# Optimization experiments

Measured on AMD Instinct MI355X. Metric: run time of the kernel, lower is better.

Reference implementation:

```python
import jax, jax.numpy as jnp
import numpy as np

B = 1048576
NUM_USERS = 200000
NUM_ITEMS = 100000
NUM_GROUPS = 50000
D = 32  # embedding_dim; grp_forward hardcodes 4*32 reshape -> 3 members per group


def setup_inputs() -> dict:
    key = jax.random.key(0)
    ks = jax.random.split(key, 12)
    return {
        "group_inputs": jax.random.randint(ks[0], (B,), 0, NUM_GROUPS, dtype=jnp.int32),
        "item_inputs": jax.random.randint(ks[1], (B,), 0, NUM_ITEMS, dtype=jnp.int32),
        "group_members": jax.random.randint(ks[2], (NUM_GROUPS, 3), 0, NUM_USERS, dtype=jnp.int32),
        "user_emb": jax.random.normal(ks[3], (NUM_USERS, D), dtype=jnp.float32) * 0.1,
        "item_emb": jax.random.normal(ks[4], (NUM_ITEMS, D), dtype=jnp.float32) * 0.1,
        "att_w1": jax.random.normal(ks[5], (4 * D, 16), dtype=jnp.float32) * 0.1,
        "att_b1": jnp.zeros((16,), dtype=jnp.float32),
        "att_w2": jax.random.normal(ks[6], (16, 3), dtype=jnp.float32) * 0.1,
        "att_b2": jnp.zeros((3,), dtype=jnp.float32),
        "pred_w1": jax.random.normal(ks[7], (3 * D, 8), dtype=jnp.float32) * 0.1,
        "pred_b1": jnp.zeros((8,), dtype=jnp.float32),
        "pred_w2": jax.random.normal(ks[8], (8, 1), dtype=jnp.float32) * 0.1,
        "pred_b2": jnp.zeros((1,), dtype=jnp.float32),
    }


def reference(group_inputs, item_inputs, group_members,
              user_emb, item_emb,
              att_w1, att_b1, att_w2, att_b2,
              pred_w1, pred_b1, pred_w2, pred_b2):
    # Vectorized form of AGREE.grp_forward (3 members per group, dropout=0 eval)
    members = group_members[group_inputs]            # [B, 3]
    me = user_emb[members]                            # [B, 3, D] member embeds
    ie = item_emb[item_inputs]                        # [B, D]
    # concat(members, item) along member dim, flatten to [B, 4D]
    x = jnp.concatenate([me.reshape(-1, 3 * D), ie], axis=1)  # [B, 4D]
    h = jax.nn.relu(x @ att_w1 + att_b1)              # [B, 16]
    wt = jax.nn.softmax(h @ att_w2 + att_b2, axis=1)  # [B, 3] attention weights
    g = jnp.einsum('bm,bmd->bd', wt, me)              # [B, D] attended group embed
    new = jnp.concatenate([g * ie, g, ie], axis=1)    # [B, 3D]
    h2 = jax.nn.relu(new @ pred_w1 + pred_b1)         # [B, 8]
    y = jax.nn.sigmoid(h2 @ pred_w2 + pred_b2)        # [B, 1]
    return y
```

## Files before the change

kernel.cpp:

```cpp
#include <hip/hip_runtime.h>
#include <math.h>
#include <stdint.h>

#define DD 32
#define GRECW 56
#define IRECW 24

__device__ __forceinline__ uint32_t bf16rne(float f) {
    uint32_t u = __float_as_uint(f);
    return (u + 0x7fffu + ((u >> 16) & 1u)) >> 16;
}
__device__ __forceinline__ uint32_t pack2(float a, float b) {
    return bf16rne(a) | (bf16rne(b) << 16);
}
#define BLO(u) __uint_as_float((u) << 16)
#define BHI(u) __uint_as_float((u) & 0xffff0000u)

__global__ __launch_bounds__(256) void grp_pre(
    const int* __restrict__ gm, const float* __restrict__ ue,
    const float* __restrict__ w1, const float* __restrict__ b1,
    uint32_t* __restrict__ grec, int NG)
{
    int tid = blockIdx.x * 256 + threadIdx.x;
    int g = tid >> 2, q = tid & 3;
    if (g >= NG) return;
    uint32_t* rec = grec + (size_t)g * GRECW;

    int u0 = gm[3 * g + 0], u1 = gm[3 * g + 1], u2 = gm[3 * g + 2];
    float me[96];
    {
        const float4* p0 = reinterpret_cast<const float4*>(ue + (size_t)u0 * DD);
        const float4* p1 = reinterpret_cast<const float4*>(ue + (size_t)u1 * DD);
        const float4* p2 = reinterpret_cast<const float4*>(ue + (size_t)u2 * DD);
        #pragma unroll
        for (int c = 0; c < 8; ++c) {
            float4 v0 = p0[c], v1 = p1[c], v2 = p2[c];
            me[4*c+0]    = v0.x; me[4*c+1]    = v0.y; me[4*c+2]    = v0.z; me[4*c+3]    = v0.w;
            me[32+4*c+0] = v1.x; me[32+4*c+1] = v1.y; me[32+4*c+2] = v1.z; me[32+4*c+3] = v1.w;
            me[64+4*c+0] = v2.x; me[64+4*c+1] = v2.y; me[64+4*c+2] = v2.z; me[64+4*c+3] = v2.w;
        }
    }
    float s0 = b1[4*q+0], s1 = b1[4*q+1], s2 = b1[4*q+2], s3 = b1[4*q+3];
    #pragma unroll
    for (int d = 0; d < 96; ++d) {
        float x = me[d];
        const float4 wv = *reinterpret_cast<const float4*>(w1 + d * 16 + 4 * q);
        s0 = fmaf(x, wv.x, s0);
        s1 = fmaf(x, wv.y, s1);
        s2 = fmaf(x, wv.z, s2);
        s3 = fmaf(x, wv.w, s3);
    }
    uint2 sw;
    sw.x = pack2(s0, s1);
    sw.y = pack2(s2, s3);
    *reinterpret_cast<uint2*>(rec + 2 * q) = sw;

    if (q >= 1) {
        int m = q - 1;
        const float* src = me + 32 * m;
        uint32_t* dst = rec + 8 + 16 * m;
        #pragma unroll
        for (int c = 0; c < 4; ++c) {
            uint4 o;
            o.x = pack2(src[8*c+0], src[8*c+1]);
            o.y = pack2(src[8*c+2], src[8*c+3]);
            o.z = pack2(src[8*c+4], src[8*c+5]);
            o.w = pack2(src[8*c+6], src[8*c+7]);
            *reinterpret_cast<uint4*>(dst + 4 * c) = o;
        }
    }
}

__global__ __launch_bounds__(256) void item_pre(
    const float* __restrict__ itemb, const float* __restrict__ w1,
    uint32_t* __restrict__ irec, int NI)
{
    int tid = blockIdx.x * 256 + threadIdx.x;
    int i = tid >> 1, q = tid & 1;
    if (i >= NI) return;
    uint32_t* rec = irec + (size_t)i * IRECW;

    float ev[32];
    {
        const float4* p = reinterpret_cast<const float4*>(itemb + (size_t)i * DD);
        #pragma unroll
        for (int c = 0; c < 8; ++c) {
            float4 v = p[c];
            ev[4*c+0] = v.x; ev[4*c+1] = v.y; ev[4*c+2] = v.z; ev[4*c+3] = v.w;
        }
    }
    float tt[8];
    #pragma unroll
    for (int j = 0; j < 8; ++j) tt[j] = 0.0f;
    #pragma unroll
    for (int d = 0; d < 32; ++d) {
        float x = ev[d];
        const float4 wa = *reinterpret_cast<const float4*>(w1 + (96 + d) * 16 + 8 * q);
        const float4 wb = *reinterpret_cast<const float4*>(w1 + (96 + d) * 16 + 8 * q + 4);
        tt[0] = fmaf(x, wa.x, tt[0]); tt[1] = fmaf(x, wa.y, tt[1]);
        tt[2] = fmaf(x, wa.z, tt[2]); tt[3] = fmaf(x, wa.w, tt[3]);
        tt[4] = fmaf(x, wb.x, tt[4]); tt[5] = fmaf(x, wb.y, tt[5]);
        tt[6] = fmaf(x, wb.z, tt[6]); tt[7] = fmaf(x, wb.w, tt[7]);
    }
    uint4 tw;
    tw.x = pack2(tt[0], tt[1]); tw.y = pack2(tt[2], tt[3]);
    tw.z = pack2(tt[4], tt[5]); tw.w = pack2(tt[6], tt[7]);
    *reinterpret_cast<uint4*>(rec + 4 * q) = tw;

    {
        const float* src = ev + 16 * q;
        uint32_t* dst = rec + 8 + 8 * q;
        #pragma unroll
        for (int c = 0; c < 2; ++c) {
            uint4 o;
            o.x = pack2(src[8*c+0], src[8*c+1]);
            o.y = pack2(src[8*c+2], src[8*c+3]);
            o.z = pack2(src[8*c+4], src[8*c+5]);
            o.w = pack2(src[8*c+6], src[8*c+7]);
            *reinterpret_cast<uint4*>(dst + 4 * c) = o;
        }
    }
}

__global__ __launch_bounds__(256) void agree_main(
    const int* __restrict__ gi, const int* __restrict__ ii,
    const uint32_t* __restrict__ grec, const uint32_t* __restrict__ irec,
    const float* __restrict__ w2, const float* __restrict__ b2,
    const float* __restrict__ pw1, const float* __restrict__ pb1,
    const float* __restrict__ pw2, const float* __restrict__ pb2,
    float* __restrict__ out, int B)
{
    int b = blockIdx.x * 256 + threadIdx.x;
    if (b >= B) return;

    const uint4* gr4 = reinterpret_cast<const uint4*>(grec + (size_t)gi[b] * GRECW);
    const uint4* ir4 = reinterpret_cast<const uint4*>(irec + (size_t)ii[b] * IRECW);

    uint4 G[14];
    #pragma unroll
    for (int c = 0; c < 14; ++c) G[c] = gr4[c];
    uint4 I[6];
    #pragma unroll
    for (int c = 0; c < 6; ++c) I[c] = ir4[c];

    float h[16];
    #pragma unroll
    for (int c = 0; c < 2; ++c) {
        uint4 sa = G[c];
        uint4 ta = I[c];
        h[8*c+0] = fmaxf(BLO(sa.x) + BLO(ta.x), 0.0f);
        h[8*c+1] = fmaxf(BHI(sa.x) + BHI(ta.x), 0.0f);
        h[8*c+2] = fmaxf(BLO(sa.y) + BLO(ta.y), 0.0f);
        h[8*c+3] = fmaxf(BHI(sa.y) + BHI(ta.y), 0.0f);
        h[8*c+4] = fmaxf(BLO(sa.z) + BLO(ta.z), 0.0f);
        h[8*c+5] = fmaxf(BHI(sa.z) + BHI(ta.z), 0.0f);
        h[8*c+6] = fmaxf(BLO(sa.w) + BLO(ta.w), 0.0f);
        h[8*c+7] = fmaxf(BHI(sa.w) + BHI(ta.w), 0.0f);
    }

    float l0 = b2[0], l1 = b2[1], l2 = b2[2];
    #pragma unroll
    for (int j = 0; j < 16; ++j) {
        l0 = fmaf(h[j], w2[j * 3 + 0], l0);
        l1 = fmaf(h[j], w2[j * 3 + 1], l1);
        l2 = fmaf(h[j], w2[j * 3 + 2], l2);
    }
    float mx = fmaxf(l0, fmaxf(l1, l2));
    float e0 = __expf(l0 - mx);
    float e1 = __expf(l1 - mx);
    float e2 = __expf(l2 - mx);
    float inv = 1.0f / (e0 + e1 + e2);
    float wt0 = e0 * inv, wt1 = e1 * inv, wt2 = e2 * inv;

    float g[32];
    #pragma unroll
    for (int c = 0; c < 4; ++c) {
        uint4 a  = G[2 + c];
        uint4 bq = G[6 + c];
        uint4 cq = G[10 + c];
        g[8*c+0] = fmaf(wt0, BLO(a.x), fmaf(wt1, BLO(bq.x), wt2 * BLO(cq.x)));
        g[8*c+1] = fmaf(wt0, BHI(a.x), fmaf(wt1, BHI(bq.x), wt2 * BHI(cq.x)));
        g[8*c+2] = fmaf(wt0, BLO(a.y), fmaf(wt1, BLO(bq.y), wt2 * BLO(cq.y)));
        g[8*c+3] = fmaf(wt0, BHI(a.y), fmaf(wt1, BHI(bq.y), wt2 * BHI(cq.y)));
        g[8*c+4] = fmaf(wt0, BLO(a.z), fmaf(wt1, BLO(bq.z), wt2 * BLO(cq.z)));
        g[8*c+5] = fmaf(wt0, BHI(a.z), fmaf(wt1, BHI(bq.z), wt2 * BHI(cq.z)));
        g[8*c+6] = fmaf(wt0, BLO(a.w), fmaf(wt1, BLO(bq.w), wt2 * BLO(cq.w)));
        g[8*c+7] = fmaf(wt0, BHI(a.w), fmaf(wt1, BHI(bq.w), wt2 * BHI(cq.w)));
    }

    float h2[8];
    #pragma unroll
    for (int j = 0; j < 8; ++j) h2[j] = pb1[j];

    #pragma unroll
    for (int c = 0; c < 4; ++c) {
        uint4 e4 = I[2 + c];
        float ef[8];
        ef[0] = BLO(e4.x); ef[1] = BHI(e4.x);
        ef[2] = BLO(e4.y); ef[3] = BHI(e4.y);
        ef[4] = BLO(e4.z); ef[5] = BHI(e4.z);
        ef[6] = BLO(e4.w); ef[7] = BHI(e4.w);
        #pragma unroll
        for (int r = 0; r < 8; ++r) {
            int d = 8 * c + r;
            float e  = ef[r];
            float gd = g[d];
            float ge = gd * e;
            #pragma unroll
            for (int j = 0; j < 8; ++j) {
                h2[j] = fmaf(ge, pw1[d * 8 + j],        h2[j]);
                h2[j] = fmaf(gd, pw1[(32 + d) * 8 + j], h2[j]);
                h2[j] = fmaf(e,  pw1[(64 + d) * 8 + j], h2[j]);
            }
        }
    }

    float z = pb2[0];
    #pragma unroll
    for (int j = 0; j < 8; ++j)
        z = fmaf(fmaxf(h2[j], 0.0f), pw2[j], z);

    out[b] = 1.0f / (1.0f + __expf(-z));
}

__global__ __launch_bounds__(256) void agree_fwd(
    const int* __restrict__ gi, const int* __restrict__ ii,
    const int* __restrict__ gm,
    const float* __restrict__ ue, const float* __restrict__ itemb,
    const float* __restrict__ w1, const float* __restrict__ b1,
    const float* __restrict__ w2, const float* __restrict__ b2,
    const float* __restrict__ pw1, const float* __restrict__ pb1,
    const float* __restrict__ pw2, const float* __restrict__ pb2,
    float* __restrict__ out, int B)
{
    int b = blockIdx.x * blockDim.x + threadIdx.x;
    if (b >= B) return;
    int g = gi[b], it = ii[b];
    int m0 = gm[3*g+0], m1 = gm[3*g+1], m2 = gm[3*g+2];
    float me[3][DD], iev[DD];
    {
        const float4* p0 = reinterpret_cast<const float4*>(ue + (size_t)m0 * DD);
        const float4* p1 = reinterpret_cast<const float4*>(ue + (size_t)m1 * DD);
        const float4* p2 = reinterpret_cast<const float4*>(ue + (size_t)m2 * DD);
        const float4* p3 = reinterpret_cast<const float4*>(itemb + (size_t)it * DD);
        #pragma unroll
        for (int c = 0; c < 8; ++c) {
            float4 v0 = p0[c], v1 = p1[c], v2 = p2[c], v3 = p3[c];
            me[0][4*c]=v0.x; me[0][4*c+1]=v0.y; me[0][4*c+2]=v0.z; me[0][4*c+3]=v0.w;
            me[1][4*c]=v1.x; me[1][4*c+1]=v1.y; me[1][4*c+2]=v1.z; me[1][4*c+3]=v1.w;
            me[2][4*c]=v2.x; me[2][4*c+1]=v2.y; me[2][4*c+2]=v2.z; me[2][4*c+3]=v2.w;
            iev[4*c]=v3.x; iev[4*c+1]=v3.y; iev[4*c+2]=v3.z; iev[4*c+3]=v3.w;
        }
    }
    float h[16];
    #pragma unroll
    for (int j = 0; j < 16; ++j) h[j] = b1[j];
    #pragma unroll
    for (int m = 0; m < 3; ++m)
        #pragma unroll
        for (int kk = 0; kk < DD; ++kk) {
            float xk = me[m][kk];
            #pragma unroll
            for (int j = 0; j < 16; ++j)
                h[j] = fmaf(xk, w1[(m*DD+kk)*16+j], h[j]);
        }
    #pragma unroll
    for (int kk = 0; kk < DD; ++kk) {
        float xk = iev[kk];
        #pragma unroll
        for (int j = 0; j < 16; ++j)
            h[j] = fmaf(xk, w1[(3*DD+kk)*16+j], h[j]);
    }
    #pragma unroll
    for (int j = 0; j < 16; ++j) h[j] = fmaxf(h[j], 0.0f);
    float l0 = b2[0], l1 = b2[1], l2 = b2[2];
    #pragma unroll
    for (int j = 0; j < 16; ++j) {
        l0 = fmaf(h[j], w2[j*3+0], l0);
        l1 = fmaf(h[j], w2[j*3+1], l1);
        l2 = fmaf(h[j], w2[j*3+2], l2);
    }
    float mx = fmaxf(l0, fmaxf(l1, l2));
    float e0 = __expf(l0-mx), e1 = __expf(l1-mx), e2 = __expf(l2-mx);
    float inv = 1.0f / (e0+e1+e2);
    float wt0 = e0*inv, wt1 = e1*inv, wt2 = e2*inv;
    float h2[8];
    #pragma unroll
    for (int j = 0; j < 8; ++j) h2[j] = pb1[j];
    #pragma unroll
    for (int d = 0; d < DD; ++d) {
        float gd  = wt0*me[0][d] + wt1*me[1][d] + wt2*me[2][d];
        float gie = gd * iev[d];
        #pragma unroll
        for (int j = 0; j < 8; ++j) {
            h2[j] = fmaf(gie,    pw1[d*8+j],          h2[j]);
            h2[j] = fmaf(gd,     pw1[(DD+d)*8+j],     h2[j]);
            h2[j] = fmaf(iev[d], pw1[(2*DD+d)*8+j],   h2[j]);
        }
    }
    float z = pb2[0];
    #pragma unroll
    for (int j = 0; j < 8; ++j)
        z = fmaf(fmaxf(h2[j], 0.0f), pw2[j], z);
    out[b] = 1.0f / (1.0f + __expf(-z));
}

extern "C" void kernel_launch(void* const* d_in, const int* in_sizes, int n_in,
                              void* d_out, int out_size, void* d_ws, size_t ws_size,
                              hipStream_t stream) {
    const int*   gi    = (const int*)d_in[0];
    const int*   ii    = (const int*)d_in[1];
    const int*   gm    = (const int*)d_in[2];
    const float* ue    = (const float*)d_in[3];
    const float* itemb = (const float*)d_in[4];
    const float* w1    = (const float*)d_in[5];
    const float* b1    = (const float*)d_in[6];
    const float* w2    = (const float*)d_in[7];
    const float* b2    = (const float*)d_in[8];
    const float* pw1   = (const float*)d_in[9];
    const float* pb1   = (const float*)d_in[10];
    const float* pw2   = (const float*)d_in[11];
    const float* pb2   = (const float*)d_in[12];
    float* out = (float*)d_out;

    int B  = in_sizes[0];
    int NG = in_sizes[2] / 3;
    int NI = in_sizes[4] / DD;

    size_t need = ((size_t)NG * GRECW + (size_t)NI * IRECW) * sizeof(uint32_t) + 512;
    if (ws_size >= need) {
        char* ws = (char*)d_ws;
        uint32_t* grec = (uint32_t*)ws;
        uint32_t* irec = grec + (((size_t)NG * GRECW + 63) & ~(size_t)63);

        hipLaunchKernelGGL(grp_pre, dim3((4 * NG + 255) / 256), dim3(256), 0, stream,
                           gm, ue, w1, b1, grec, NG);
        hipLaunchKernelGGL(item_pre, dim3((2 * NI + 255) / 256), dim3(256), 0, stream,
                           itemb, w1, irec, NI);
        hipLaunchKernelGGL(agree_main, dim3((B + 255) / 256), dim3(256), 0, stream,
                           gi, ii, grec, irec, w2, b2, pw1, pb1, pw2, pb2, out, B);
    } else {
        hipLaunchKernelGGL(agree_fwd, dim3((B + 255) / 256), dim3(256), 0, stream,
                           gi, ii, gm, ue, itemb, w1, b1, w2, b2,
                           pw1, pb1, pw2, pb2, out, B);
    }
}
```

Before: 250.0 us.

## Split-K precompute with shuffle reduction and two rows per thread in main kernel

The group and item precompute kernels now split the input dimension across the 4 lanes of a quad, so each lane loads only its slice of the embeddings, computes partial 16-wide sums and reduces them with xor-shuffles. This removes redundant embedding gathers and lowers per-thread register pressure. The main kernel processes two batch rows per thread, issuing both sets of record gathers before computing, to raise memory-level parallelism. The cost is higher register use in the main kernel, which may reduce occupancy, and extra shuffle work in the precompute.

```diff
diff --git a/kernel.cpp b/kernel.cpp
--- a/kernel.cpp
+++ b/kernel.cpp
@@ -15,6 +15,14 @@
 }
 #define BLO(u) __uint_as_float((u) << 16)
 #define BHI(u) __uint_as_float((u) & 0xffff0000u)
+
+__device__ __forceinline__ void pick4(const float* s, int q,
+                                      float& r0, float& r1, float& r2, float& r3) {
+    if (q == 0)      { r0 = s[0];  r1 = s[1];  r2 = s[2];  r3 = s[3];  }
+    else if (q == 1) { r0 = s[4];  r1 = s[5];  r2 = s[6];  r3 = s[7];  }
+    else if (q == 2) { r0 = s[8];  r1 = s[9];  r2 = s[10]; r3 = s[11]; }
+    else             { r0 = s[12]; r1 = s[13]; r2 = s[14]; r3 = s[15]; }
+}
 
 __global__ __launch_bounds__(256) void grp_pre(
     const int* __restrict__ gm, const float* __restrict__ ue,
@@ -27,47 +35,59 @@
     uint32_t* rec = grec + (size_t)g * GRECW;
 
     int u0 = gm[3 * g + 0], u1 = gm[3 * g + 1], u2 = gm[3 * g + 2];
-    float me[96];
-    {
-        const float4* p0 = reinterpret_cast<const float4*>(ue + (size_t)u0 * DD);
-        const float4* p1 = reinterpret_cast<const float4*>(ue + (size_t)u1 * DD);
-        const float4* p2 = reinterpret_cast<const float4*>(ue + (size_t)u2 * DD);
-        #pragma unroll
-        for (int c = 0; c < 8; ++c) {
-            float4 v0 = p0[c], v1 = p1[c], v2 = p2[c];
-            me[4*c+0]    = v0.x; me[4*c+1]    = v0.y; me[4*c+2]    = v0.z; me[4*c+3]    = v0.w;
-            me[32+4*c+0] = v1.x; me[32+4*c+1] = v1.y; me[32+4*c+2] = v1.z; me[32+4*c+3] = v1.w;
-            me[64+4*c+0] = v2.x; me[64+4*c+1] = v2.y; me[64+4*c+2] = v2.z; me[64+4*c+3] = v2.w;
-        }
-    }
-    float s0 = b1[4*q+0], s1 = b1[4*q+1], s2 = b1[4*q+2], s3 = b1[4*q+3];
-    #pragma unroll
-    for (int d = 0; d < 96; ++d) {
-        float x = me[d];
-        const float4 wv = *reinterpret_cast<const float4*>(w1 + d * 16 + 4 * q);
-        s0 = fmaf(x, wv.x, s0);
-        s1 = fmaf(x, wv.y, s1);
-        s2 = fmaf(x, wv.z, s2);
-        s3 = fmaf(x, wv.w, s3);
-    }
+
+    float x[24];
+    #pragma unroll
+    for (int c = 0; c < 6; ++c) {
+        int c4 = 6 * q + c;
+        int m  = c4 >> 3;
+        int s4 = c4 & 7;
+        int uu = (m == 0) ? u0 : ((m == 1) ? u1 : u2);
+        float4 v = reinterpret_cast<const float4*>(ue + (size_t)uu * DD)[s4];
+        x[4*c+0] = v.x; x[4*c+1] = v.y; x[4*c+2] = v.z; x[4*c+3] = v.w;
+    }
+
+    float s[16];
+    #pragma unroll
+    for (int j = 0; j < 16; ++j) s[j] = 0.0f;
+    #pragma unroll
+    for (int k = 0; k < 24; ++k) {
+        int d = 24 * q + k;
+        const float4* wr = reinterpret_cast<const float4*>(w1 + d * 16);
+        float4 w0 = wr[0], w1v = wr[1], w2v = wr[2], w3v = wr[3];
+        float xv = x[k];
+        s[0]  = fmaf(xv, w0.x,  s[0]);  s[1]  = fmaf(xv, w0.y,  s[1]);
+        s[2]  = fmaf(xv, w0.z,  s[2]);  s[3]  = fmaf(xv, w0.w,  s[3]);
+        s[4]  = fmaf(xv, w1v.x, s[4]);  s[5]  = fmaf(xv, w1v.y, s[5]);
+        s[6]  = fmaf(xv, w1v.z, s[6]);  s[7]  = fmaf(xv, w1v.w, s[7]);
+        s[8]  = fmaf(xv, w2v.x, s[8]);  s[9]  = fmaf(xv, w2v.y, s[9]);
+        s[10] = fmaf(xv, w2v.z, s[10]); s[11] = fmaf(xv, w2v.w, s[11]);
+        s[12] = fmaf(xv, w3v.x, s[12]); s[13] = fmaf(xv, w3v.y, s[13]);
+        s[14] = fmaf(xv, w3v.z, s[14]); s[15] = fmaf(xv, w3v.w, s[15]);
+    }
+    #pragma unroll
+    for (int j = 0; j < 16; ++j) {
+        s[j] += __shfl_xor(s[j], 1, 64);
+        s[j] += __shfl_xor(s[j], 2, 64);
+    }
+
+    float r0, r1, r2, r3;
+    pick4(s, q, r0, r1, r2, r3);
+    const float* bp = b1 + 4 * q;
     uint2 sw;
-    sw.x = pack2(s0, s1);
-    sw.y = pack2(s2, s3);
+    sw.x = pack2(r0 + bp[0], r1 + bp[1]);
+    sw.y = pack2(r2 + bp[2], r3 + bp[3]);
     *reinterpret_cast<uint2*>(rec + 2 * q) = sw;
 
-    if (q >= 1) {
-        int m = q - 1;
-        const float* src = me + 32 * m;
-        uint32_t* dst = rec + 8 + 16 * m;
-        #pragma unroll
-        for (int c = 0; c < 4; ++c) {
-            uint4 o;
-            o.x = pack2(src[8*c+0], src[8*c+1]);
-            o.y = pack2(src[8*c+2], src[8*c+3]);
-            o.z = pack2(src[8*c+4], src[8*c+5]);
-            o.w = pack2(src[8*c+6], src[8*c+7]);
-            *reinterpret_cast<uint4*>(dst + 4 * c) = o;
-        }
+    uint32_t* dst = rec + 8 + 12 * q;
+    #pragma unroll
+    for (int c = 0; c < 3; ++c) {
+        uint4 o;
+        o.x = pack2(x[8*c+0], x[8*c+1]);
+        o.y = pack2(x[8*c+2], x[8*c+3]);
+        o.z = pack2(x[8*c+4], x[8*c+5]);
+        o.w = pack2(x[8*c+6], x[8*c+7]);
+        *reinterpret_cast<uint4*>(dst + 4 * c) = o;
     }
 }
 
@@ -76,73 +96,63 @@
     uint32_t* __restrict__ irec, int NI)
 {
     int tid = blockIdx.x * 256 + threadIdx.x;
-    int i = tid >> 1, q = tid & 1;
+    int i = tid >> 2, q = tid & 3;
     if (i >= NI) return;
     uint32_t* rec = irec + (size_t)i * IRECW;
 
-    float ev[32];
+    float x[8];
     {
-        const float4* p = reinterpret_cast<const float4*>(itemb + (size_t)i * DD);
-        #pragma unroll
-        for (int c = 0; c < 8; ++c) {
-            float4 v = p[c];
-            ev[4*c+0] = v.x; ev[4*c+1] = v.y; ev[4*c+2] = v.z; ev[4*c+3] = v.w;
-        }
-    }
-    float tt[8];
-    #pragma unroll
-    for (int j = 0; j < 8; ++j) tt[j] = 0.0f;
-    #pragma unroll
-    for (int d = 0; d < 32; ++d) {
-        float x = ev[d];
-        const float4 wa = *reinterpret_cast<const float4*>(w1 + (96 + d) * 16 + 8 * q);
-        const float4 wb = *reinterpret_cast<const float4*>(w1 + (96 + d) * 16 + 8 * q + 4);
-        tt[0] = fmaf(x, wa.x, tt[0]); tt[1] = fmaf(x, wa.y, tt[1]);
-        tt[2] = fmaf(x, wa.z, tt[2]); tt[3] = fmaf(x, wa.w, tt[3]);
-        tt[4] = fmaf(x, wb.x, tt[4]); tt[5] = fmaf(x, wb.y, tt[5]);
-        tt[6] = fmaf(x, wb.z, tt[6]); tt[7] = fmaf(x, wb.w, tt[7]);
-    }
-    uint4 tw;
-    tw.x = pack2(tt[0], tt[1]); tw.y = pack2(tt[2], tt[3]);
-    tw.z = pack2(tt[4], tt[5]); tw.w = pack2(tt[6], tt[7]);
-    *reinterpret_cast<uint4*>(rec + 4 * q) = tw;
-
-    {
-        const float* src = ev + 16 * q;
-        uint32_t* dst = rec + 8 + 8 * q;
-        #pragma unroll
-        for (int c = 0; c < 2; ++c) {
-            uint4 o;
-            o.x = pack2(src[8*c+0], src[8*c+1]);
-            o.y = pack2(src[8*c+2], src[8*c+3]);
-            o.z = pack2(src[8*c+4], src[8*c+5]);
-            o.w = pack2(src[8*c+6], src[8*c+7]);
-            *reinterpret_cast<uint4*>(dst + 4 * c) = o;
-        }
-    }
-}
-
-__global__ __launch_bounds__(256) void agree_main(
-    const int* __restrict__ gi, const int* __restrict__ ii,
-    const uint32_t* __restrict__ grec, const uint32_t* __restrict__ irec,
+        const float4* p = reinterpret_cast<const float4*>(itemb + (size_t)i * DD) + 2 * q;
+        float4 v0 = p[0], v1 = p[1];
+        x[0] = v0.x; x[1] = v0.y; x[2] = v0.z; x[3] = v0.w;
+        x[4] = v1.x; x[5] = v1.y; x[6] = v1.z; x[7] = v1.w;
+    }
+
+    float t[16];
+    #pragma unroll
+    for (int j = 0; j < 16; ++j) t[j] = 0.0f;
+    #pragma unroll
+    for (int k = 0; k < 8; ++k) {
+        int d = 8 * q + k;
+        const float4* wr = reinterpret_cast<const float4*>(w1 + (96 + d) * 16);
+        float4 w0 = wr[0], w1v = wr[1], w2v = wr[2], w3v = wr[3];
+        float xv = x[k];
+        t[0]  = fmaf(xv, w0.x,  t[0]);  t[1]  = fmaf(xv, w0.y,  t[1]);
+        t[2]  = fmaf(xv, w0.z,  t[2]);  t[3]  = fmaf(xv, w0.w,  t[3]);
+        t[4]  = fmaf(xv, w1v.x, t[4]);  t[5]  = fmaf(xv, w1v.y, t[5]);
+        t[6]  = fmaf(xv, w1v.z, t[6]);  t[7]  = fmaf(xv, w1v.w, t[7]);
+        t[8]  = fmaf(xv, w2v.x, t[8]);  t[9]  = fmaf(xv, w2v.y, t[9]);
+        t[10] = fmaf(xv, w2v.z, t[10]); t[11] = fmaf(xv, w2v.w, t[11]);
+        t[12] = fmaf(xv, w3v.x, t[12]); t[13] = fmaf(xv, w3v.y, t[13]);
+        t[14] = fmaf(xv, w3v.z, t[14]); t[15] = fmaf(xv, w3v.w, t[15]);
+    }
+    #pragma unroll
+    for (int j = 0; j < 16; ++j) {
+        t[j] += __shfl_xor(t[j], 1, 64);
+        t[j] += __shfl_xor(t[j], 2, 64);
+    }
+
+    float r0, r1, r2, r3;
+    pick4(t, q, r0, r1, r2, r3);
+    uint2 tw;
+    tw.x = pack2(r0, r1);
+    tw.y = pack2(r2, r3);
+    *reinterpret_cast<uint2*>(rec + 2 * q) = tw;
+
+    uint4 o;
+    o.x = pack2(x[0], x[1]);
+    o.y = pack2(x[2], x[3]);
+    o.z = pack2(x[4], x[5]);
+    o.w = pack2(x[6], x[7]);
+    *reinterpret_cast<uint4*>(rec + 8 + 4 * q) = o;
+}
+
+__device__ __forceinline__ float agree_eval(
+    const uint4* G, const uint4* I,
     const float* __restrict__ w2, const float* __restrict__ b2,
     const float* __restrict__ pw1, const float* __restrict__ pb1,
-    const float* __restrict__ pw2, const float* __restrict__ pb2,
-    float* __restrict__ out, int B)
-{
-    int b = blockIdx.x * 256 + threadIdx.x;
-    if (b >= B) return;
-
-    const uint4* gr4 = reinterpret_cast<const uint4*>(grec + (size_t)gi[b] * GRECW);
-    const uint4* ir4 = reinterpret_cast<const uint4*>(irec + (size_t)ii[b] * IRECW);
-
-    uint4 G[14];
-    #pragma unroll
-    for (int c = 0; c < 14; ++c) G[c] = gr4[c];
-    uint4 I[6];
-    #pragma unroll
-    for (int c = 0; c < 6; ++c) I[c] = ir4[c];
-
+    const float* __restrict__ pw2, const float* __restrict__ pb2)
+{
     float h[16];
     #pragma unroll
     for (int c = 0; c < 2; ++c) {
@@ -220,7 +230,45 @@
     for (int j = 0; j < 8; ++j)
         z = fmaf(fmaxf(h2[j], 0.0f), pw2[j], z);
 
-    out[b] = 1.0f / (1.0f + __expf(-z));
+    return 1.0f / (1.0f + __expf(-z));
+}
+
+__global__ __launch_bounds__(256) void agree_main(
+    const int* __restrict__ gi, const int* __restrict__ ii,
+    const uint32_t* __restrict__ grec, const uint32_t* __restrict__ irec,
+    const float* __restrict__ w2, const float* __restrict__ b2,
+    const float* __restrict__ pw1, const float* __restrict__ pb1,
+    const float* __restrict__ pw2, const float* __restrict__ pb2,
+    float* __restrict__ out, int B)
+{
+    int t = blockIdx.x * 256 + threadIdx.x;
+    int half = (B + 1) >> 1;
+    if (t >= half) return;
+    int b0 = t;
+    int b1i = t + half;
+    bool has1 = (b1i < B);
+
+    const uint4* gr0 = reinterpret_cast<const uint4*>(grec + (size_t)gi[b0] * GRECW);
+    const uint4* ir0 = reinterpret_cast<const uint4*>(irec + (size_t)ii[b0] * IRECW);
+    int g1 = gi[has1 ? b1i : b0];
+    int i1 = ii[has1 ? b1i : b0];
+    const uint4* gr1 = reinterpret_cast<const uint4*>(grec + (size_t)g1 * GRECW);
+    const uint4* ir1 = reinterpret_cast<const uint4*>(irec + (size_t)i1 * IRECW);
+
+    uint4 G0[14], I0[6];
+    #pragma unroll
+    for (int c = 0; c < 14; ++c) G0[c] = gr0[c];
+    #pragma unroll
+    for (int c = 0; c < 6; ++c)  I0[c] = ir0[c];
+    uint4 G1[14], I1[6];
+    #pragma unroll
+    for (int c = 0; c < 14; ++c) G1[c] = gr1[c];
+    #pragma unroll
+    for (int c = 0; c < 6; ++c)  I1[c] = ir1[c];
+
+    out[b0] = agree_eval(G0, I0, w2, b2, pw1, pb1, pw2, pb2);
+    float y1 = agree_eval(G1, I1, w2, b2, pw1, pb1, pw2, pb2);
+    if (has1) out[b1i] = y1;
 }
 
 __global__ __launch_bounds__(256) void agree_fwd(
@@ -335,9 +383,10 @@
 
         hipLaunchKernelGGL(grp_pre, dim3((4 * NG + 255) / 256), dim3(256), 0, stream,
                            gm, ue, w1, b1, grec, NG);
-        hipLaunchKernelGGL(item_pre, dim3((2 * NI + 255) / 256), dim3(256), 0, stream,
+        hipLaunchKernelGGL(item_pre, dim3((4 * NI + 255) / 256), dim3(256), 0, stream,
                            itemb, w1, irec, NI);
-        hipLaunchKernelGGL(agree_main, dim3((B + 255) / 256), dim3(256), 0, stream,
+        int half = (B + 1) >> 1;
+        hipLaunchKernelGGL(agree_main, dim3((half + 255) / 256), dim3(256), 0, stream,
                            gi, ii, grec, irec, w2, b2, pw1, pb1, pw2, pb2, out, B);
     } else {
         hipLaunchKernelGGL(agree_fwd, dim3((B + 255) / 256), dim3(256), 0, stream,
```

Measured after the change: 277.4 us. 1.11x slower.

## Shrink precomputed group/item records with fp8 storage and folded linear terms

Applied to the files above, without the earlier changes.

The two precompute kernels are merged into a single launch. The linear parts of the prediction MLP, the g and ie contributions, are moved into precompute: per-member pw1 projections and the item pw1 projection are stored as bf16. Member and item embeddings and the item attention partial are stored as fp8 using hardware cvt_pk builtins when available. This shrinks the per-sample gathered record from 80 to 64 dwords and removes many FMAs in the main kernel, at the cost of larger quantization error from fp8 storage.

```diff
diff --git a/kernel.cpp b/kernel.cpp
--- a/kernel.cpp
+++ b/kernel.cpp
@@ -3,8 +3,8 @@
 #include <stdint.h>
 
 #define DD 32
-#define GRECW 56
-#define IRECW 24
+#define GRECW 48
+#define IRECW 16
 
 __device__ __forceinline__ uint32_t bf16rne(float f) {
     uint32_t u = __float_as_uint(f);
@@ -16,109 +16,240 @@
 #define BLO(u) __uint_as_float((u) << 16)
 #define BHI(u) __uint_as_float((u) & 0xffff0000u)
 
-__global__ __launch_bounds__(256) void grp_pre(
+__device__ inline uint32_t sw_enc(float f) {
+    float af = fabsf(f);
+    uint32_t s = (__float_as_uint(f) >> 24) & 0x80u;
+    if (!(af >= 0.015625f)) {
+        int m = (int)rintf(af * 512.0f);
+        if (m > 7) return s | 0x08u;
+        return s | (uint32_t)m;
+    }
+    if (af >= 448.0f) return s | 0x7eu;
+    int e; float fr = frexpf(af, &e);
+    int M = (int)rintf(fr * 16.0f) - 8;
+    int E = e + 6;
+    if (M == 8) { M = 0; E += 1; }
+    return s | ((uint32_t)E << 3) | (uint32_t)M;
+}
+__device__ inline float sw_dec(uint32_t b) {
+    uint32_t em = b & 0x7fu;
+    float v = (em < 8) ? (float)em * (1.0f / 512.0f)
+                       : ldexpf((float)(8 + (em & 7)), (int)(em >> 3) - 10);
+    return (b & 0x80u) ? -v : v;
+}
+
+typedef float f32x2 __attribute__((ext_vector_type(2)));
+
+__device__ __forceinline__ uint32_t enc4(float a, float b, float c, float d) {
+#if __has_builtin(__builtin_amdgcn_cvt_pk_fp8_f32)
+    int v = 0;
+    v = __builtin_amdgcn_cvt_pk_fp8_f32(a, b, v, false);
+    v = __builtin_amdgcn_cvt_pk_fp8_f32(c, d, v, true);
+    return (uint32_t)v;
+#else
+    return sw_enc(a) | (sw_enc(b) << 8) | (sw_enc(c) << 16) | (sw_enc(d) << 24);
+#endif
+}
+__device__ __forceinline__ void dec4(uint32_t w, float& o0, float& o1, float& o2, float& o3) {
+#if __has_builtin(__builtin_amdgcn_cvt_pk_f32_fp8)
+    f32x2 lo = __builtin_amdgcn_cvt_pk_f32_fp8((int)w, false);
+    f32x2 hi = __builtin_amdgcn_cvt_pk_f32_fp8((int)w, true);
+    o0 = lo.x; o1 = lo.y; o2 = hi.x; o3 = hi.y;
+#else
+    o0 = sw_dec(w & 255u); o1 = sw_dec((w >> 8) & 255u);
+    o2 = sw_dec((w >> 16) & 255u); o3 = sw_dec(w >> 24);
+#endif
+}
+
+__global__ __launch_bounds__(256) void pre_all(
     const int* __restrict__ gm, const float* __restrict__ ue,
+    const float* __restrict__ itemb,
     const float* __restrict__ w1, const float* __restrict__ b1,
-    uint32_t* __restrict__ grec, int NG)
+    const float* __restrict__ pw1,
+    uint32_t* __restrict__ grec, uint32_t* __restrict__ irec,
+    int NG, int NI, int GBLK)
 {
-    int tid = blockIdx.x * 256 + threadIdx.x;
-    int g = tid >> 2, q = tid & 3;
-    if (g >= NG) return;
-    uint32_t* rec = grec + (size_t)g * GRECW;
-
-    int u0 = gm[3 * g + 0], u1 = gm[3 * g + 1], u2 = gm[3 * g + 2];
-    float me[96];
-    {
-        const float4* p0 = reinterpret_cast<const float4*>(ue + (size_t)u0 * DD);
-        const float4* p1 = reinterpret_cast<const float4*>(ue + (size_t)u1 * DD);
-        const float4* p2 = reinterpret_cast<const float4*>(ue + (size_t)u2 * DD);
-        #pragma unroll
-        for (int c = 0; c < 8; ++c) {
-            float4 v0 = p0[c], v1 = p1[c], v2 = p2[c];
-            me[4*c+0]    = v0.x; me[4*c+1]    = v0.y; me[4*c+2]    = v0.z; me[4*c+3]    = v0.w;
-            me[32+4*c+0] = v1.x; me[32+4*c+1] = v1.y; me[32+4*c+2] = v1.z; me[32+4*c+3] = v1.w;
-            me[64+4*c+0] = v2.x; me[64+4*c+1] = v2.y; me[64+4*c+2] = v2.z; me[64+4*c+3] = v2.w;
-        }
-    }
-    float s0 = b1[4*q+0], s1 = b1[4*q+1], s2 = b1[4*q+2], s3 = b1[4*q+3];
-    #pragma unroll
-    for (int d = 0; d < 96; ++d) {
-        float x = me[d];
-        const float4 wv = *reinterpret_cast<const float4*>(w1 + d * 16 + 4 * q);
-        s0 = fmaf(x, wv.x, s0);
-        s1 = fmaf(x, wv.y, s1);
-        s2 = fmaf(x, wv.z, s2);
-        s3 = fmaf(x, wv.w, s3);
-    }
-    uint2 sw;
-    sw.x = pack2(s0, s1);
-    sw.y = pack2(s2, s3);
-    *reinterpret_cast<uint2*>(rec + 2 * q) = sw;
-
-    if (q >= 1) {
-        int m = q - 1;
-        const float* src = me + 32 * m;
-        uint32_t* dst = rec + 8 + 16 * m;
-        #pragma unroll
-        for (int c = 0; c < 4; ++c) {
+    if ((int)blockIdx.x < GBLK) {
+        int tid = blockIdx.x * 256 + threadIdx.x;
+        int g = tid >> 2, q = tid & 3;
+        if (g >= NG) return;
+        uint32_t* rec = grec + (size_t)g * GRECW;
+        int u0 = gm[3 * g + 0], u1 = gm[3 * g + 1], u2 = gm[3 * g + 2];
+
+        float x0[8], x1[8], x2[8];
+        {
+            const float4* p = reinterpret_cast<const float4*>(ue + (size_t)u0 * DD) + 2 * q;
+            float4 a = p[0], b = p[1];
+            x0[0]=a.x; x0[1]=a.y; x0[2]=a.z; x0[3]=a.w; x0[4]=b.x; x0[5]=b.y; x0[6]=b.z; x0[7]=b.w;
+        }
+        {
+            const float4* p = reinterpret_cast<const float4*>(ue + (size_t)u1 * DD) + 2 * q;
+            float4 a = p[0], b = p[1];
+            x1[0]=a.x; x1[1]=a.y; x1[2]=a.z; x1[3]=a.w; x1[4]=b.x; x1[5]=b.y; x1[6]=b.z; x1[7]=b.w;
+        }
+        {
+            const float4* p = reinterpret_cast<const float4*>(ue + (size_t)u2 * DD) + 2 * q;
+            float4 a = p[0], b = p[1];
+            x2[0]=a.x; x2[1]=a.y; x2[2]=a.z; x2[3]=a.w; x2[4]=b.x; x2[5]=b.y; x2[6]=b.z; x2[7]=b.w;
+        }
+
+        float s[16]; float P0[8], P1[8], P2[8];
+        #pragma unroll
+        for (int j = 0; j < 16; ++j) s[j] = 0.0f;
+        #pragma unroll
+        for (int j = 0; j < 8; ++j) { P0[j] = 0.0f; P1[j] = 0.0f; P2[j] = 0.0f; }
+
+        #pragma unroll
+        for (int k = 0; k < 8; ++k) {
+            int dm = 8 * q + k;
+            const float4* br = reinterpret_cast<const float4*>(pw1 + (DD + dm) * 8);
+            float4 B0 = br[0], B1 = br[1];
+            {
+                const float4* wr = reinterpret_cast<const float4*>(w1 + (0 * DD + dm) * 16);
+                float4 wa = wr[0], wb = wr[1], wc = wr[2], wd = wr[3];
+                float xv = x0[k];
+                s[0]=fmaf(xv,wa.x,s[0]); s[1]=fmaf(xv,wa.y,s[1]); s[2]=fmaf(xv,wa.z,s[2]); s[3]=fmaf(xv,wa.w,s[3]);
+                s[4]=fmaf(xv,wb.x,s[4]); s[5]=fmaf(xv,wb.y,s[5]); s[6]=fmaf(xv,wb.z,s[6]); s[7]=fmaf(xv,wb.w,s[7]);
+                s[8]=fmaf(xv,wc.x,s[8]); s[9]=fmaf(xv,wc.y,s[9]); s[10]=fmaf(xv,wc.z,s[10]); s[11]=fmaf(xv,wc.w,s[11]);
+                s[12]=fmaf(xv,wd.x,s[12]); s[13]=fmaf(xv,wd.y,s[13]); s[14]=fmaf(xv,wd.z,s[14]); s[15]=fmaf(xv,wd.w,s[15]);
+                P0[0]=fmaf(xv,B0.x,P0[0]); P0[1]=fmaf(xv,B0.y,P0[1]); P0[2]=fmaf(xv,B0.z,P0[2]); P0[3]=fmaf(xv,B0.w,P0[3]);
+                P0[4]=fmaf(xv,B1.x,P0[4]); P0[5]=fmaf(xv,B1.y,P0[5]); P0[6]=fmaf(xv,B1.z,P0[6]); P0[7]=fmaf(xv,B1.w,P0[7]);
+            }
+            {
+                const float4* wr = reinterpret_cast<const float4*>(w1 + (1 * DD + dm) * 16);
+                float4 wa = wr[0], wb = wr[1], wc = wr[2], wd = wr[3];
+                float xv = x1[k];
+                s[0]=fmaf(xv,wa.x,s[0]); s[1]=fmaf(xv,wa.y,s[1]); s[2]=fmaf(xv,wa.z,s[2]); s[3]=fmaf(xv,wa.w,s[3]);
+                s[4]=fmaf(xv,wb.x,s[4]); s[5]=fmaf(xv,wb.y,s[5]); s[6]=fmaf(xv,wb.z,s[6]); s[7]=fmaf(xv,wb.w,s[7]);
+                s[8]=fmaf(xv,wc.x,s[8]); s[9]=fmaf(xv,wc.y,s[9]); s[10]=fmaf(xv,wc.z,s[10]); s[11]=fmaf(xv,wc.w,s[11]);
+                s[12]=fmaf(xv,wd.x,s[12]); s[13]=fmaf(xv,wd.y,s[13]); s[14]=fmaf(xv,wd.z,s[14]); s[15]=fmaf(xv,wd.w,s[15]);
+                P1[0]=fmaf(xv,B0.x,P1[0]); P1[1]=fmaf(xv,B0.y,P1[1]); P1[2]=fmaf(xv,B0.z,P1[2]); P1[3]=fmaf(xv,B0.w,P1[3]);
+                P1[4]=fmaf(xv,B1.x,P1[4]); P1[5]=fmaf(xv,B1.y,P1[5]); P1[6]=fmaf(xv,B1.z,P1[6]); P1[7]=fmaf(xv,B1.w,P1[7]);
+            }
+            {
+                const float4* wr = reinterpret_cast<const float4*>(w1 + (2 * DD + dm) * 16);
+                float4 wa = wr[0], wb = wr[1], wc = wr[2], wd = wr[3];
+                float xv = x2[k];
+                s[0]=fmaf(xv,wa.x,s[0]); s[1]=fmaf(xv,wa.y,s[1]); s[2]=fmaf(xv,wa.z,s[2]); s[3]=fmaf(xv,wa.w,s[3]);
+                s[4]=fmaf(xv,wb.x,s[4]); s[5]=fmaf(xv,wb.y,s[5]); s[6]=fmaf(xv,wb.z,s[6]); s[7]=fmaf(xv,wb.w,s[7]);
+                s[8]=fmaf(xv,wc.x,s[8]); s[9]=fmaf(xv,wc.y,s[9]); s[10]=fmaf(xv,wc.z,s[10]); s[11]=fmaf(xv,wc.w,s[11]);
+                s[12]=fmaf(xv,wd.x,s[12]); s[13]=fmaf(xv,wd.y,s[13]); s[14]=fmaf(xv,wd.z,s[14]); s[15]=fmaf(xv,wd.w,s[15]);
+                P2[0]=fmaf(xv,B0.x,P2[0]); P2[1]=fmaf(xv,B0.y,P2[1]); P2[2]=fmaf(xv,B0.z,P2[2]); P2[3]=fmaf(xv,B0.w,P2[3]);
+                P2[4]=fmaf(xv,B1.x,P2[4]); P2[5]=fmaf(xv,B1.y,P2[5]); P2[6]=fmaf(xv,B1.z,P2[6]); P2[7]=fmaf(xv,B1.w,P2[7]);
+            }
+        }
+
+        #pragma unroll
+        for (int j = 0; j < 16; ++j) {
+            s[j] += __shfl_xor(s[j], 1, 64);
+            s[j] += __shfl_xor(s[j], 2, 64);
+        }
+        #pragma unroll
+        for (int j = 0; j < 8; ++j) {
+            P0[j] += __shfl_xor(P0[j], 1, 64); P0[j] += __shfl_xor(P0[j], 2, 64);
+            P1[j] += __shfl_xor(P1[j], 1, 64); P1[j] += __shfl_xor(P1[j], 2, 64);
+            P2[j] += __shfl_xor(P2[j], 1, 64); P2[j] += __shfl_xor(P2[j], 2, 64);
+        }
+
+        if (q == 0) {
             uint4 o;
-            o.x = pack2(src[8*c+0], src[8*c+1]);
-            o.y = pack2(src[8*c+2], src[8*c+3]);
-            o.z = pack2(src[8*c+4], src[8*c+5]);
-            o.w = pack2(src[8*c+6], src[8*c+7]);
-            *reinterpret_cast<uint4*>(dst + 4 * c) = o;
-        }
-    }
-}
-
-__global__ __launch_bounds__(256) void item_pre(
-    const float* __restrict__ itemb, const float* __restrict__ w1,
-    uint32_t* __restrict__ irec, int NI)
-{
-    int tid = blockIdx.x * 256 + threadIdx.x;
-    int i = tid >> 1, q = tid & 1;
-    if (i >= NI) return;
-    uint32_t* rec = irec + (size_t)i * IRECW;
-
-    float ev[32];
-    {
-        const float4* p = reinterpret_cast<const float4*>(itemb + (size_t)i * DD);
-        #pragma unroll
-        for (int c = 0; c < 8; ++c) {
-            float4 v = p[c];
-            ev[4*c+0] = v.x; ev[4*c+1] = v.y; ev[4*c+2] = v.z; ev[4*c+3] = v.w;
-        }
-    }
-    float tt[8];
-    #pragma unroll
-    for (int j = 0; j < 8; ++j) tt[j] = 0.0f;
-    #pragma unroll
-    for (int d = 0; d < 32; ++d) {
-        float x = ev[d];
-        const float4 wa = *reinterpret_cast<const float4*>(w1 + (96 + d) * 16 + 8 * q);
-        const float4 wb = *reinterpret_cast<const float4*>(w1 + (96 + d) * 16 + 8 * q + 4);
-        tt[0] = fmaf(x, wa.x, tt[0]); tt[1] = fmaf(x, wa.y, tt[1]);
-        tt[2] = fmaf(x, wa.z, tt[2]); tt[3] = fmaf(x, wa.w, tt[3]);
-        tt[4] = fmaf(x, wb.x, tt[4]); tt[5] = fmaf(x, wb.y, tt[5]);
-        tt[6] = fmaf(x, wb.z, tt[6]); tt[7] = fmaf(x, wb.w, tt[7]);
-    }
-    uint4 tw;
-    tw.x = pack2(tt[0], tt[1]); tw.y = pack2(tt[2], tt[3]);
-    tw.z = pack2(tt[4], tt[5]); tw.w = pack2(tt[6], tt[7]);
-    *reinterpret_cast<uint4*>(rec + 4 * q) = tw;
-
-    {
-        const float* src = ev + 16 * q;
-        uint32_t* dst = rec + 8 + 8 * q;
-        #pragma unroll
-        for (int c = 0; c < 2; ++c) {
+            o.x = pack2(s[0] + b1[0],  s[1] + b1[1]);
+            o.y = pack2(s[2] + b1[2],  s[3] + b1[3]);
+            o.z = pack2(s[4] + b1[4],  s[5] + b1[5]);
+            o.w = pack2(s[6] + b1[6],  s[7] + b1[7]);
+            *reinterpret_cast<uint4*>(rec + 0) = o;
+            uint4 o2;
+            o2.x = pack2(s[8] + b1[8],   s[9] + b1[9]);
+            o2.y = pack2(s[10] + b1[10], s[11] + b1[11]);
+            o2.z = pack2(s[12] + b1[12], s[13] + b1[13]);
+            o2.w = pack2(s[14] + b1[14], s[15] + b1[15]);
+            *reinterpret_cast<uint4*>(rec + 4) = o2;
+        } else if (q == 1) {
             uint4 o;
-            o.x = pack2(src[8*c+0], src[8*c+1]);
-            o.y = pack2(src[8*c+2], src[8*c+3]);
-            o.z = pack2(src[8*c+4], src[8*c+5]);
-            o.w = pack2(src[8*c+6], src[8*c+7]);
-            *reinterpret_cast<uint4*>(dst + 4 * c) = o;
-        }
+            o.x = pack2(P0[0], P0[1]); o.y = pack2(P0[2], P0[3]);
+            o.z = pack2(P0[4], P0[5]); o.w = pack2(P0[6], P0[7]);
+            *reinterpret_cast<uint4*>(rec + 8) = o;
+            uint4 o2;
+            o2.x = pack2(P1[0], P1[1]); o2.y = pack2(P1[2], P1[3]);
+            o2.z = pack2(P1[4], P1[5]); o2.w = pack2(P1[6], P1[7]);
+            *reinterpret_cast<uint4*>(rec + 12) = o2;
+        } else if (q == 2) {
+            uint4 o;
+            o.x = pack2(P2[0], P2[1]); o.y = pack2(P2[2], P2[3]);
+            o.z = pack2(P2[4], P2[5]); o.w = pack2(P2[6], P2[7]);
+            *reinterpret_cast<uint4*>(rec + 16) = o;
+        }
+        uint2 w;
+        w.x = enc4(x0[0], x0[1], x0[2], x0[3]);
+        w.y = enc4(x0[4], x0[5], x0[6], x0[7]);
+        *reinterpret_cast<uint2*>(rec + 20 + 2 * q) = w;
+        w.x = enc4(x1[0], x1[1], x1[2], x1[3]);
+        w.y = enc4(x1[4], x1[5], x1[6], x1[7]);
+        *reinterpret_cast<uint2*>(rec + 28 + 2 * q) = w;
+        w.x = enc4(x2[0], x2[1], x2[2], x2[3]);
+        w.y = enc4(x2[4], x2[5], x2[6], x2[7]);
+        *reinterpret_cast<uint2*>(rec + 36 + 2 * q) = w;
+    } else {
+        int tid = (blockIdx.x - GBLK) * 256 + threadIdx.x;
+        int i = tid >> 2, q = tid & 3;
+        if (i >= NI) return;
+        uint32_t* rec = irec + (size_t)i * IRECW;
+
+        float y[8];
+        {
+            const float4* p = reinterpret_cast<const float4*>(itemb + (size_t)i * DD) + 2 * q;
+            float4 a = p[0], b = p[1];
+            y[0]=a.x; y[1]=a.y; y[2]=a.z; y[3]=a.w; y[4]=b.x; y[5]=b.y; y[6]=b.z; y[7]=b.w;
+        }
+        float t[16], Q[8];
+        #pragma unroll
+        for (int j = 0; j < 16; ++j) t[j] = 0.0f;
+        #pragma unroll
+        for (int j = 0; j < 8; ++j) Q[j] = 0.0f;
+
+        #pragma unroll
+        for (int k = 0; k < 8; ++k) {
+            int dm = 8 * q + k;
+            const float4* wr = reinterpret_cast<const float4*>(w1 + (96 + dm) * 16);
+            float4 wa = wr[0], wb = wr[1], wc = wr[2], wd = wr[3];
+            const float4* cr = reinterpret_cast<const float4*>(pw1 + (2 * DD + dm) * 8);
+            float4 C0 = cr[0], C1 = cr[1];
+            float xv = y[k];
+            t[0]=fmaf(xv,wa.x,t[0]); t[1]=fmaf(xv,wa.y,t[1]); t[2]=fmaf(xv,wa.z,t[2]); t[3]=fmaf(xv,wa.w,t[3]);
+            t[4]=fmaf(xv,wb.x,t[4]); t[5]=fmaf(xv,wb.y,t[5]); t[6]=fmaf(xv,wb.z,t[6]); t[7]=fmaf(xv,wb.w,t[7]);
+            t[8]=fmaf(xv,wc.x,t[8]); t[9]=fmaf(xv,wc.y,t[9]); t[10]=fmaf(xv,wc.z,t[10]); t[11]=fmaf(xv,wc.w,t[11]);
+            t[12]=fmaf(xv,wd.x,t[12]); t[13]=fmaf(xv,wd.y,t[13]); t[14]=fmaf(xv,wd.z,t[14]); t[15]=fmaf(xv,wd.w,t[15]);
+            Q[0]=fmaf(xv,C0.x,Q[0]); Q[1]=fmaf(xv,C0.y,Q[1]); Q[2]=fmaf(xv,C0.z,Q[2]); Q[3]=fmaf(xv,C0.w,Q[3]);
+            Q[4]=fmaf(xv,C1.x,Q[4]); Q[5]=fmaf(xv,C1.y,Q[5]); Q[6]=fmaf(xv,C1.z,Q[6]); Q[7]=fmaf(xv,C1.w,Q[7]);
+        }
+        #pragma unroll
+        for (int j = 0; j < 16; ++j) {
+            t[j] += __shfl_xor(t[j], 1, 64);
+            t[j] += __shfl_xor(t[j], 2, 64);
+        }
+        #pragma unroll
+        for (int j = 0; j < 8; ++j) {
+            Q[j] += __shfl_xor(Q[j], 1, 64);
+            Q[j] += __shfl_xor(Q[j], 2, 64);
+        }
+
+        if (q == 0) {
+            uint4 o;
+            o.x = enc4(t[0], t[1], t[2], t[3]);
+            o.y = enc4(t[4], t[5], t[6], t[7]);
+            o.z = enc4(t[8], t[9], t[10], t[11]);
+            o.w = enc4(t[12], t[13], t[14], t[15]);
+            *reinterpret_cast<uint4*>(rec + 0) = o;
+        } else if (q == 1) {
+            uint4 o;
+            o.x = pack2(Q[0], Q[1]); o.y = pack2(Q[2], Q[3]);
+            o.z = pack2(Q[4], Q[5]); o.w = pack2(Q[6], Q[7]);
+            *reinterpret_cast<uint4*>(rec + 4) = o;
+        }
+        uint2 w;
+        w.x = enc4(y[0], y[1], y[2], y[3]);
+        w.y = enc4(y[4], y[5], y[6], y[7]);
+        *reinterpret_cast<uint2*>(rec + 8 + 2 * q) = w;
     }
 }
 
@@ -136,27 +267,33 @@
     const uint4* gr4 = reinterpret_cast<const uint4*>(grec + (size_t)gi[b] * GRECW);
     const uint4* ir4 = reinterpret_cast<const uint4*>(irec + (size_t)ii[b] * IRECW);
 
-    uint4 G[14];
-    #pragma unroll
-    for (int c = 0; c < 14; ++c) G[c] = gr4[c];
-    uint4 I[6];
-    #pragma unroll
-    for (int c = 0; c < 6; ++c) I[c] = ir4[c];
-
+    uint4 G0 = gr4[0], G1 = gr4[1], G2 = gr4[2], G3 = gr4[3], G4 = gr4[4];
+    uint4 G5 = gr4[5], G6 = gr4[6], G7 = gr4[7], G8 = gr4[8], G9 = gr4[9], G10 = gr4[10];
+    uint4 I0 = ir4[0], I1 = ir4[1], I2 = ir4[2], I3 = ir4[3];
+    __builtin_amdgcn_sched_barrier(0);
+
+    float tt[16];
+    dec4(I0.x, tt[0], tt[1], tt[2], tt[3]);
+    dec4(I0.y, tt[4], tt[5], tt[6], tt[7]);
+    dec4(I0.z, tt[8], tt[9], tt[10], tt[11]);
+    dec4(I0.w, tt[12], tt[13], tt[14], tt[15]);
     float h[16];
-    #pragma unroll
-    for (int c = 0; c < 2; ++c) {
-        uint4 sa = G[c];
-        uint4 ta = I[c];
-        h[8*c+0] = fmaxf(BLO(sa.x) + BLO(ta.x), 0.0f);
-        h[8*c+1] = fmaxf(BHI(sa.x) + BHI(ta.x), 0.0f);
-        h[8*c+2] = fmaxf(BLO(sa.y) + BLO(ta.y), 0.0f);
-        h[8*c+3] = fmaxf(BHI(sa.y) + BHI(ta.y), 0.0f);
-        h[8*c+4] = fmaxf(BLO(sa.z) + BLO(ta.z), 0.0f);
-        h[8*c+5] = fmaxf(BHI(sa.z) + BHI(ta.z), 0.0f);
-        h[8*c+6] = fmaxf(BLO(sa.w) + BLO(ta.w), 0.0f);
-        h[8*c+7] = fmaxf(BHI(sa.w) + BHI(ta.w), 0.0f);
-    }
+    h[0]  = fmaxf(BLO(G0.x) + tt[0],  0.0f);
+    h[1]  = fmaxf(BHI(G0.x) + tt[1],  0.0f);
+    h[2]  = fmaxf(BLO(G0.y) + tt[2],  0.0f);
+    h[3]  = fmaxf(BHI(G0.y) + tt[3],  0.0f);
+    h[4]  = fmaxf(BLO(G0.z) + tt[4],  0.0f);
+    h[5]  = fmaxf(BHI(G0.z) + tt[5],  0.0f);
+    h[6]  = fmaxf(BLO(G0.w) + tt[6],  0.0f);
+    h[7]  = fmaxf(BHI(G0.w) + tt[7],  0.0f);
+    h[8]  = fmaxf(BLO(G1.x) + tt[8],  0.0f);
+    h[9]  = fmaxf(BHI(G1.x) + tt[9],  0.0f);
+    h[10] = fmaxf(BLO(G1.y) + tt[10], 0.0f);
+    h[11] = fmaxf(BHI(G1.y) + tt[11], 0.0f);
+    h[12] = fmaxf(BLO(G1.z) + tt[12], 0.0f);
+    h[13] = fmaxf(BHI(G1.z) + tt[13], 0.0f);
+    h[14] = fmaxf(BLO(G1.w) + tt[14], 0.0f);
+    h[15] = fmaxf(BHI(G1.w) + tt[15], 0.0f);
 
     float l0 = b2[0], l1 = b2[1], l2 = b2[2];
     #pragma unroll
@@ -172,48 +309,50 @@
     float inv = 1.0f / (e0 + e1 + e2);
     float wt0 = e0 * inv, wt1 = e1 * inv, wt2 = e2 * inv;
 
-    float g[32];
-    #pragma unroll
-    for (int c = 0; c < 4; ++c) {
-        uint4 a  = G[2 + c];
-        uint4 bq = G[6 + c];
-        uint4 cq = G[10 + c];
-        g[8*c+0] = fmaf(wt0, BLO(a.x), fmaf(wt1, BLO(bq.x), wt2 * BLO(cq.x)));
-        g[8*c+1] = fmaf(wt0, BHI(a.x), fmaf(wt1, BHI(bq.x), wt2 * BHI(cq.x)));
-        g[8*c+2] = fmaf(wt0, BLO(a.y), fmaf(wt1, BLO(bq.y), wt2 * BLO(cq.y)));
-        g[8*c+3] = fmaf(wt0, BHI(a.y), fmaf(wt1, BHI(bq.y), wt2 * BHI(cq.y)));
-        g[8*c+4] = fmaf(wt0, BLO(a.z), fmaf(wt1, BLO(bq.z), wt2 * BLO(cq.z)));
-        g[8*c+5] = fmaf(wt0, BHI(a.z), fmaf(wt1, BHI(bq.z), wt2 * BHI(cq.z)));
-        g[8*c+6] = fmaf(wt0, BLO(a.w), fmaf(wt1, BLO(bq.w), wt2 * BLO(cq.w)));
-        g[8*c+7] = fmaf(wt0, BHI(a.w), fmaf(wt1, BHI(bq.w), wt2 * BHI(cq.w)));
-    }
-
     float h2[8];
-    #pragma unroll
-    for (int j = 0; j < 8; ++j) h2[j] = pb1[j];
-
-    #pragma unroll
-    for (int c = 0; c < 4; ++c) {
-        uint4 e4 = I[2 + c];
-        float ef[8];
-        ef[0] = BLO(e4.x); ef[1] = BHI(e4.x);
-        ef[2] = BLO(e4.y); ef[3] = BHI(e4.y);
-        ef[4] = BLO(e4.z); ef[5] = BHI(e4.z);
-        ef[6] = BLO(e4.w); ef[7] = BHI(e4.w);
-        #pragma unroll
-        for (int r = 0; r < 8; ++r) {
-            int d = 8 * c + r;
-            float e  = ef[r];
-            float gd = g[d];
-            float ge = gd * e;
-            #pragma unroll
-            for (int j = 0; j < 8; ++j) {
-                h2[j] = fmaf(ge, pw1[d * 8 + j],        h2[j]);
-                h2[j] = fmaf(gd, pw1[(32 + d) * 8 + j], h2[j]);
-                h2[j] = fmaf(e,  pw1[(64 + d) * 8 + j], h2[j]);
-            }
-        }
-    }
+    h2[0] = pb1[0] + BLO(I1.x); h2[1] = pb1[1] + BHI(I1.x);
+    h2[2] = pb1[2] + BLO(I1.y); h2[3] = pb1[3] + BHI(I1.y);
+    h2[4] = pb1[4] + BLO(I1.z); h2[5] = pb1[5] + BHI(I1.z);
+    h2[6] = pb1[6] + BLO(I1.w); h2[7] = pb1[7] + BHI(I1.w);
+    {
+        float p0[8], p1[8], p2[8];
+        p0[0]=BLO(G2.x); p0[1]=BHI(G2.x); p0[2]=BLO(G2.y); p0[3]=BHI(G2.y);
+        p0[4]=BLO(G2.z); p0[5]=BHI(G2.z); p0[6]=BLO(G2.w); p0[7]=BHI(G2.w);
+        p1[0]=BLO(G3.x); p1[1]=BHI(G3.x); p1[2]=BLO(G3.y); p1[3]=BHI(G3.y);
+        p1[4]=BLO(G3.z); p1[5]=BHI(G3.z); p1[6]=BLO(G3.w); p1[7]=BHI(G3.w);
+        p2[0]=BLO(G4.x); p2[1]=BHI(G4.x); p2[2]=BLO(G4.y); p2[3]=BHI(G4.y);
+        p2[4]=BLO(G4.z); p2[5]=BHI(G4.z); p2[6]=BLO(G4.w); p2[7]=BHI(G4.w);
+        #pragma unroll
+        for (int j = 0; j < 8; ++j)
+            h2[j] = fmaf(wt0, p0[j], fmaf(wt1, p1[j], fmaf(wt2, p2[j], h2[j])));
+    }
+
+#define DO_CHUNK(DBASE, w00, w01, w10, w11, w20, w21, we0, we1)                 \
+    {                                                                           \
+        float m0[8], m1[8], m2[8], ee[8];                                       \
+        dec4(w00, m0[0], m0[1], m0[2], m0[3]);                                  \
+        dec4(w01, m0[4], m0[5], m0[6], m0[7]);                                  \
+        dec4(w10, m1[0], m1[1], m1[2], m1[3]);                                  \
+        dec4(w11, m1[4], m1[5], m1[6], m1[7]);                                  \
+        dec4(w20, m2[0], m2[1], m2[2], m2[3]);                                  \
+        dec4(w21, m2[4], m2[5], m2[6], m2[7]);                                  \
+        dec4(we0, ee[0], ee[1], ee[2], ee[3]);                                  \
+        dec4(we1, ee[4], ee[5], ee[6], ee[7]);                                  \
+        _Pragma("unroll")                                                       \
+        for (int r = 0; r < 8; ++r) {                                           \
+            float gd = fmaf(wt0, m0[r], fmaf(wt1, m1[r], wt2 * m2[r]));         \
+            float ge = gd * ee[r];                                              \
+            const float* arow = pw1 + (DBASE + r) * 8;                          \
+            _Pragma("unroll")                                                   \
+            for (int j = 0; j < 8; ++j) h2[j] = fmaf(ge, arow[j], h2[j]);       \
+        }                                                                       \
+    }
+
+    DO_CHUNK(0,  G5.x, G5.y, G7.x, G7.y, G9.x,  G9.y,  I2.x, I2.y)
+    DO_CHUNK(8,  G5.z, G5.w, G7.z, G7.w, G9.z,  G9.w,  I2.z, I2.w)
+    DO_CHUNK(16, G6.x, G6.y, G8.x, G8.y, G10.x, G10.y, I3.x, I3.y)
+    DO_CHUNK(24, G6.z, G6.w, G8.z, G8.w, G10.z, G10.w, I3.z, I3.w)
+#undef DO_CHUNK
 
     float z = pb2[0];
     #pragma unroll
@@ -327,16 +466,18 @@
     int NG = in_sizes[2] / 3;
     int NI = in_sizes[4] / DD;
 
-    size_t need = ((size_t)NG * GRECW + (size_t)NI * IRECW) * sizeof(uint32_t) + 512;
+    size_t gbytes = ((size_t)NG * GRECW * 4 + 255) & ~(size_t)255;
+    size_t ibytes = (size_t)NI * IRECW * 4;
+    size_t need = gbytes + ibytes + 256;
     if (ws_size >= need) {
         char* ws = (char*)d_ws;
         uint32_t* grec = (uint32_t*)ws;
-        uint32_t* irec = grec + (((size_t)NG * GRECW + 63) & ~(size_t)63);
-
-        hipLaunchKernelGGL(grp_pre, dim3((4 * NG + 255) / 256), dim3(256), 0, stream,
-                           gm, ue, w1, b1, grec, NG);
-        hipLaunchKernelGGL(item_pre, dim3((2 * NI + 255) / 256), dim3(256), 0, stream,
-                           itemb, w1, irec, NI);
+        uint32_t* irec = (uint32_t*)(ws + gbytes);
+
+        int GBLK = (4 * NG + 255) / 256;
+        int IBLK = (4 * NI + 255) / 256;
+        hipLaunchKernelGGL(pre_all, dim3(GBLK + IBLK), dim3(256), 0, stream,
+                           gm, ue, itemb, w1, b1, pw1, grec, irec, NG, NI, GBLK);
         hipLaunchKernelGGL(agree_main, dim3((B + 255) / 256), dim3(256), 0, stream,
                            gi, ii, grec, irec, w2, b2, pw1, pb1, pw2, pb2, out, B);
     } else {
```

Result: faster. 230.1 us (-8.0%).
